# Performance work log

Measured on AMD Instinct MI355X. Metric: run time of the kernel, lower is better.

## Reference

```python
import jax, jax.numpy as jnp
import numpy as np


def setup_inputs() -> dict:
    key = jax.random.key(0)
    k1, k2 = jax.random.split(key)
    shape = (4, 16, 4000, 400)  # [batch, shot, nt, nrec]
    shot_syn = jax.random.normal(k1, shape, dtype=jnp.float32)
    shot_obs = jax.random.normal(k2, shape, dtype=jnp.float32)
    return {"shot_syn": shot_syn, "shot_obs": shot_obs}


def reference(shot_syn, shot_obs):
    # Zero-mean global correlation misfit (obj_option == 4), vectorized over
    # (batch, shot). Per-shot means are taken over the (nt, nrec) plane.
    mean_pred = jnp.mean(shot_syn, axis=(2, 3), keepdims=True)
    mean_true = jnp.mean(shot_obs, axis=(2, 3), keepdims=True)
    d_pred = shot_syn - mean_pred
    d_true = shot_obs - mean_true
    # Per-shot reductions: cross term and energies, each [batch, shot].
    cross = jnp.sum(d_true * d_pred, axis=(2, 3))
    E_true = jnp.sum(d_true * d_true, axis=(2, 3))
    E_pred = jnp.sum(d_pred * d_pred, axis=(2, 3))
    # Note sum(corr_plane)/(sqrt(E_true)*sqrt(E_pred)) == cross / denom.
    loss = -jnp.sum(cross / (jnp.sqrt(E_true) * jnp.sqrt(E_pred)))
    return loss
```

## Files before the change

kernel.cpp:

```cpp
#include <hip/hip_runtime.h>
#include <math.h>

#define PLANE_ELEMS 1600000
#define NPLANES     64
#define BPP         32
#define THREADS     256

__global__ __launch_bounds__(THREADS)
void fwi_partials(const float* __restrict__ syn,
                  const float* __restrict__ obs,
                  double* __restrict__ ws)
{
    const int plane = blockIdx.x / BPP;
    const int bip   = blockIdx.x % BPP;
    const int n4    = PLANE_ELEMS / 4;

    const float4* s4 = reinterpret_cast<const float4*>(syn) + (size_t)plane * n4;
    const float4* o4 = reinterpret_cast<const float4*>(obs) + (size_t)plane * n4;

    double s_s = 0.0, s_o = 0.0, s_ss = 0.0, s_oo = 0.0, s_so = 0.0;

    #pragma unroll 2
    for (int i = bip * THREADS + threadIdx.x; i < n4; i += BPP * THREADS) {
        float4 a = s4[i];
        float4 b = o4[i];
        double a0 = a.x, a1 = a.y, a2 = a.z, a3 = a.w;
        double b0 = b.x, b1 = b.y, b2 = b.z, b3 = b.w;

        s_s += (a0 + a1) + (a2 + a3);
        s_o += (b0 + b1) + (b2 + b3);
        s_ss = fma(a0, a0, s_ss); s_ss = fma(a1, a1, s_ss);
        s_ss = fma(a2, a2, s_ss); s_ss = fma(a3, a3, s_ss);
        s_oo = fma(b0, b0, s_oo); s_oo = fma(b1, b1, s_oo);
        s_oo = fma(b2, b2, s_oo); s_oo = fma(b3, b3, s_oo);
        s_so = fma(a0, b0, s_so); s_so = fma(a1, b1, s_so);
        s_so = fma(a2, b2, s_so); s_so = fma(a3, b3, s_so);
    }

    #pragma unroll
    for (int off = 32; off > 0; off >>= 1) {
        s_s  += __shfl_down(s_s,  off);
        s_o  += __shfl_down(s_o,  off);
        s_ss += __shfl_down(s_ss, off);
        s_oo += __shfl_down(s_oo, off);
        s_so += __shfl_down(s_so, off);
    }

    __shared__ double sm[THREADS / 64][5];
    const int wave = threadIdx.x >> 6;
    const int lane = threadIdx.x & 63;
    if (lane == 0) {
        sm[wave][0] = s_s;  sm[wave][1] = s_o;
        sm[wave][2] = s_ss; sm[wave][3] = s_oo; sm[wave][4] = s_so;
    }
    __syncthreads();

    if (threadIdx.x == 0) {
        double t0 = 0, t1 = 0, t2 = 0, t3 = 0, t4 = 0;
        #pragma unroll
        for (int w = 0; w < THREADS / 64; ++w) {
            t0 += sm[w][0]; t1 += sm[w][1]; t2 += sm[w][2];
            t3 += sm[w][3]; t4 += sm[w][4];
        }
        atomicAdd(&ws[plane * 5 + 0], t0);
        atomicAdd(&ws[plane * 5 + 1], t1);
        atomicAdd(&ws[plane * 5 + 2], t2);
        atomicAdd(&ws[plane * 5 + 3], t3);
        atomicAdd(&ws[plane * 5 + 4], t4);
    }
}

__global__ __launch_bounds__(64)
void fwi_final(const double* __restrict__ ws, float* __restrict__ out)
{
    const double N = (double)PLANE_ELEMS;
    const int p = threadIdx.x;

    double Ss  = ws[p * 5 + 0];
    double So  = ws[p * 5 + 1];
    double Sss = ws[p * 5 + 2];
    double Soo = ws[p * 5 + 3];
    double Sso = ws[p * 5 + 4];

    double cross = Sso - Ss * So / N;
    double Ep    = Sss - Ss * Ss / N;
    double Et    = Soo - So * So / N;
    double term  = cross / (sqrt(Et) * sqrt(Ep));

    #pragma unroll
    for (int off = 32; off > 0; off >>= 1)
        term += __shfl_down(term, off);

    if (p == 0)
        out[0] = (float)(-term);
}

extern "C" void kernel_launch(void* const* d_in, const int* in_sizes, int n_in,
                              void* d_out, int out_size, void* d_ws, size_t ws_size,
                              hipStream_t stream)
{
    const float* syn = (const float*)d_in[0];
    const float* obs = (const float*)d_in[1];
    float* out       = (float*)d_out;
    double* ws       = (double*)d_ws;

    hipMemsetAsync(ws, 0, NPLANES * 5 * sizeof(double), stream);

    fwi_partials<<<NPLANES * BPP, THREADS, 0, stream>>>(syn, obs, ws);
    fwi_final<<<1, 64, 0, stream>>>(ws, out);
}
```

Measured before the change: 155.7 us.

## Use contiguous per-block chunks and write partials instead of atomics and memset

```diff
diff --git a/kernel.cpp b/kernel.cpp
--- a/kernel.cpp
+++ b/kernel.cpp
@@ -5,23 +5,26 @@
 #define NPLANES     64
 #define BPP         32
 #define THREADS     256
+#define N4          (PLANE_ELEMS / 4)
+#define CHUNK       (N4 / BPP)
 
 __global__ __launch_bounds__(THREADS)
 void fwi_partials(const float* __restrict__ syn,
                   const float* __restrict__ obs,
                   double* __restrict__ ws)
 {
-    const int plane = blockIdx.x / BPP;
-    const int bip   = blockIdx.x % BPP;
-    const int n4    = PLANE_ELEMS / 4;
+    const int plane = blockIdx.x >> 5;
+    const int bip   = blockIdx.x & (BPP - 1);
 
-    const float4* s4 = reinterpret_cast<const float4*>(syn) + (size_t)plane * n4;
-    const float4* o4 = reinterpret_cast<const float4*>(obs) + (size_t)plane * n4;
+    const float4* s4 = reinterpret_cast<const float4*>(syn)
+                       + (size_t)plane * N4 + (size_t)bip * CHUNK;
+    const float4* o4 = reinterpret_cast<const float4*>(obs)
+                       + (size_t)plane * N4 + (size_t)bip * CHUNK;
 
     double s_s = 0.0, s_o = 0.0, s_ss = 0.0, s_oo = 0.0, s_so = 0.0;
 
-    #pragma unroll 2
-    for (int i = bip * THREADS + threadIdx.x; i < n4; i += BPP * THREADS) {
+    #pragma unroll 4
+    for (int i = threadIdx.x; i < CHUNK; i += THREADS) {
         float4 a = s4[i];
         float4 b = o4[i];
         double a0 = a.x, a1 = a.y, a2 = a.z, a3 = a.w;
@@ -62,37 +65,53 @@
             t0 += sm[w][0]; t1 += sm[w][1]; t2 += sm[w][2];
             t3 += sm[w][3]; t4 += sm[w][4];
         }
-        atomicAdd(&ws[plane * 5 + 0], t0);
-        atomicAdd(&ws[plane * 5 + 1], t1);
-        atomicAdd(&ws[plane * 5 + 2], t2);
-        atomicAdd(&ws[plane * 5 + 3], t3);
-        atomicAdd(&ws[plane * 5 + 4], t4);
+        double* r = ws + (size_t)blockIdx.x * 5;
+        r[0] = t0; r[1] = t1; r[2] = t2; r[3] = t3; r[4] = t4;
     }
 }
 
-__global__ __launch_bounds__(64)
+__global__ __launch_bounds__(256)
 void fwi_final(const double* __restrict__ ws, float* __restrict__ out)
 {
-    const double N = (double)PLANE_ELEMS;
-    const int p = threadIdx.x;
+    const int t = threadIdx.x;
+    const int p = t & 63;
+    const int q = t >> 6;
 
-    double Ss  = ws[p * 5 + 0];
-    double So  = ws[p * 5 + 1];
-    double Sss = ws[p * 5 + 2];
-    double Soo = ws[p * 5 + 3];
-    double Sso = ws[p * 5 + 4];
+    double acc0 = 0, acc1 = 0, acc2 = 0, acc3 = 0, acc4 = 0;
+    #pragma unroll
+    for (int b = 0; b < BPP / 4; ++b) {
+        const double* r = ws + (size_t)((p * BPP) + (q * (BPP / 4)) + b) * 5;
+        acc0 += r[0]; acc1 += r[1]; acc2 += r[2]; acc3 += r[3]; acc4 += r[4];
+    }
 
-    double cross = Sso - Ss * So / N;
-    double Ep    = Sss - Ss * Ss / N;
-    double Et    = Soo - So * So / N;
-    double term  = cross / (sqrt(Et) * sqrt(Ep));
+    __shared__ double sm[4][64][5];
+    sm[q][p][0] = acc0; sm[q][p][1] = acc1; sm[q][p][2] = acc2;
+    sm[q][p][3] = acc3; sm[q][p][4] = acc4;
+    __syncthreads();
 
-    #pragma unroll
-    for (int off = 32; off > 0; off >>= 1)
-        term += __shfl_down(term, off);
+    if (t < 64) {
+        double Ss = 0, So = 0, Sss = 0, Soo = 0, Sso = 0;
+        #pragma unroll
+        for (int qq = 0; qq < 4; ++qq) {
+            Ss  += sm[qq][p][0];
+            So  += sm[qq][p][1];
+            Sss += sm[qq][p][2];
+            Soo += sm[qq][p][3];
+            Sso += sm[qq][p][4];
+        }
+        const double N = (double)PLANE_ELEMS;
+        double cross = Sso - Ss * So / N;
+        double Ep    = Sss - Ss * Ss / N;
+        double Et    = Soo - So * So / N;
+        double term  = cross / (sqrt(Et) * sqrt(Ep));
 
-    if (p == 0)
-        out[0] = (float)(-term);
+        #pragma unroll
+        for (int off = 32; off > 0; off >>= 1)
+            term += __shfl_down(term, off);
+
+        if (p == 0)
+            out[0] = (float)(-term);
+    }
 }
 
 extern "C" void kernel_launch(void* const* d_in, const int* in_sizes, int n_in,
@@ -104,8 +123,6 @@
     float* out       = (float*)d_out;
     double* ws       = (double*)d_ws;
 
-    hipMemsetAsync(ws, 0, NPLANES * 5 * sizeof(double), stream);
-
     fwi_partials<<<NPLANES * BPP, THREADS, 0, stream>>>(syn, obs, ws);
-    fwi_final<<<1, 64, 0, stream>>>(ws, out);
+    fwi_final<<<1, 256, 0, stream>>>(ws, out);
 }
```

Result: faster. 151.7 us (-2.6%).
